# Kernel tuning notes

Hardware: AMD Instinct MI355X
Metric: run time of the kernel (lower is better)

The kernel has to match this reference:

```python
import jax, jax.numpy as jnp
import numpy as np

DIM_MODEL = 1024
NUM_HEADS = 16
DROPOUT_P = 0.5
SCALE = float(np.sqrt(DIM_MODEL // NUM_HEADS))  # NOTE: source MULTIPLIES by this (unusual but faithful)
DROP_KEY = jax.random.key(42)


def setup_inputs() -> dict:
    key = jax.random.key(0)
    ks = jax.random.split(key, 9)
    B, LQ, LK, D = 4, 2048, 2048, DIM_MODEL
    s = 1.0 / np.sqrt(D)
    return {
        "query": jax.random.normal(ks[0], (B, LQ, D), jnp.float32),
        "key": jax.random.normal(ks[1], (B, LK, D), jnp.float32),
        "value": jax.random.normal(ks[2], (B, LK, D), jnp.float32),
        "Wq": jax.random.normal(ks[3], (D, D), jnp.float32) * s,
        "bq": jax.random.normal(ks[4], (D,), jnp.float32) * s,
        "Wk": jax.random.normal(ks[5], (D, D), jnp.float32) * s,
        "bk": jax.random.normal(ks[6], (D,), jnp.float32) * s,
        "Wv": jax.random.normal(ks[7], (D, D), jnp.float32) * s,
        "bv": jax.random.normal(ks[8], (D,), jnp.float32) * s,
    }


def reference(query, key, value, Wq, bq, Wk, bk, Wv, bv):
    # Linear projections (W stored as [in, out])
    q = jnp.einsum('bqd,de->bqe', query, Wq) + bq
    k = jnp.einsum('bkd,de->bke', key, Wk) + bk
    v = jnp.einsum('bkd,de->bke', value, Wv) + bv
    # scores scaled by MULTIPLYING sqrt(d_head), per source
    scores = jnp.einsum('bqe,bke->bqk', q, k) * SCALE
    probs = jax.nn.softmax(scores, axis=-1)
    # dropout (train mode, p=0.5), deterministic fixed key for reproducibility
    keep = jax.random.bernoulli(DROP_KEY, 1.0 - DROPOUT_P, probs.shape)
    probs = jnp.where(keep, probs / (1.0 - DROPOUT_P), 0.0)
    return jnp.einsum('bqk,bke->bqe', probs, v)
```

## Files before the change

kernel.cpp:

```cpp
#include <hip/hip_runtime.h>
#include <math.h>

#define BATCH  4
#define LSEQ   2048
#define DMODEL 1024
#define MROWS  (BATCH * LSEQ)
#define SCORE_SCALE 8.0f

#define THREEFRY_PARTITIONABLE 1

typedef __bf16 bf16_t;
typedef bf16_t bf16x8 __attribute__((ext_vector_type(8)));
typedef bf16_t bf16x4 __attribute__((ext_vector_type(4)));
typedef float  f32x4  __attribute__((ext_vector_type(4)));

#define LDSP(p) ((__attribute__((address_space(3))) void*)(p))
#define GLBP(p) ((const __attribute__((address_space(1))) void*)(p))

__device__ __forceinline__ unsigned rotl32(unsigned x, int r) {
    return (x << r) | (x >> (32 - r));
}

__device__ __forceinline__ void threefry2x32(unsigned k0, unsigned k1,
                                             unsigned x0, unsigned x1,
                                             unsigned& o0, unsigned& o1) {
    const unsigned ks0 = k0, ks1 = k1, ks2 = k0 ^ k1 ^ 0x1BD11BDAu;
    x0 += ks0; x1 += ks1;
#define TF_R(r) { x0 += x1; x1 = rotl32(x1, r); x1 ^= x0; }
    TF_R(13) TF_R(15) TF_R(26) TF_R(6)
    x0 += ks1; x1 += ks2 + 1u;
    TF_R(17) TF_R(29) TF_R(16) TF_R(24)
    x0 += ks2; x1 += ks0 + 2u;
    TF_R(13) TF_R(15) TF_R(26) TF_R(6)
    x0 += ks0; x1 += ks1 + 3u;
    TF_R(17) TF_R(29) TF_R(16) TF_R(24)
    x0 += ks1; x1 += ks2 + 4u;
    TF_R(13) TF_R(15) TF_R(26) TF_R(6)
    x0 += ks2; x1 += ks0 + 5u;
#undef TF_R
    o0 = x0; o1 = x1;
}

__device__ __forceinline__ bool dropout_keep(unsigned n) {
    unsigned o0, o1;
#if THREEFRY_PARTITIONABLE
    threefry2x32(0u, 42u, 0u, n, o0, o1);
    unsigned bits = o0 ^ o1;
#else
    const unsigned HALF = (unsigned)(BATCH * LSEQ) * (unsigned)LSEQ / 2u;
    unsigned c0 = (n < HALF) ? n : (n - HALF);
    unsigned c1 = (n < HALF) ? (n + HALF) : n;
    threefry2x32(0u, 42u, c0, c1, o0, o1);
    unsigned bits = (n < HALF) ? o0 : o1;
#endif
    return bits < 0x80000000u;
}

__global__ __launch_bounds__(256)
void split_f32(const float* __restrict__ X0, const float* __restrict__ X1,
               bf16_t* __restrict__ hi, bf16_t* __restrict__ lo, int n) {
    const int y = blockIdx.y;
    const float* X = y ? X1 : X0;
    long long i = (long long)(blockIdx.x * 256 + threadIdx.x) * 4;
    if (i >= n) return;
    float4 v = *(const float4*)(X + i);
    bf16x4 h, l;
    h[0] = (bf16_t)v.x; l[0] = (bf16_t)(v.x - (float)h[0]);
    h[1] = (bf16_t)v.y; l[1] = (bf16_t)(v.y - (float)h[1]);
    h[2] = (bf16_t)v.z; l[2] = (bf16_t)(v.z - (float)h[2]);
    h[3] = (bf16_t)v.w; l[3] = (bf16_t)(v.w - (float)h[3]);
    *(bf16x4*)(hi + (long long)y * n + i) = h;
    *(bf16x4*)(lo + (long long)y * n + i) = l;
}

__global__ __launch_bounds__(256)
void cvt_bf16(const float* __restrict__ X, bf16_t* __restrict__ Y, int n) {
    long long i = (long long)(blockIdx.x * 256 + threadIdx.x) * 8;
    if (i >= n) return;
    float4 a = *(const float4*)(X + i);
    float4 b = *(const float4*)(X + i + 4);
    bf16x8 o;
    o[0] = (bf16_t)a.x; o[1] = (bf16_t)a.y; o[2] = (bf16_t)a.z; o[3] = (bf16_t)a.w;
    o[4] = (bf16_t)b.x; o[5] = (bf16_t)b.y; o[6] = (bf16_t)b.z; o[7] = (bf16_t)b.w;
    *(bf16x8*)(Y + i) = o;
}

__global__ __launch_bounds__(256)
void split_transpose(const float* __restrict__ W0, const float* __restrict__ W1,
                     bf16_t* __restrict__ Th, bf16_t* __restrict__ Tl,
                     int Kd, int Nd) {
    __shared__ float t[32][33];
    const int z = blockIdx.z;
    const float* W = z ? W1 : W0;
    const long long zo = (long long)z * Kd * Nd;
    const int bx = blockIdx.x * 32;
    const int by = blockIdx.y * 32;
    const int tx = threadIdx.x & 31, ty = threadIdx.x >> 5;
#pragma unroll
    for (int i = 0; i < 4; ++i)
        t[ty + i * 8][tx] = W[(long long)(by + ty + i * 8) * Nd + bx + tx];
    __syncthreads();
#pragma unroll
    for (int i = 0; i < 4; ++i) {
        float v = t[tx][ty + i * 8];
        long long idx = zo + (long long)(bx + ty + i * 8) * Kd + by + tx;
        bf16_t h = (bf16_t)v;
        Th[idx] = h;
        Tl[idx] = (bf16_t)(v - (float)h);
    }
}

template <int SPLIT, int OUT, int BROW>
__global__ __launch_bounds__(256)
void gemm_mfma(const bf16_t* __restrict__ Ah, const bf16_t* __restrict__ Al,
               const bf16_t* __restrict__ Bh, const bf16_t* __restrict__ Bl,
               const float* __restrict__ bias, const float* __restrict__ bias2,
               float* __restrict__ Cf, bf16_t* __restrict__ Ch,
               bf16_t* __restrict__ Cl,
               int M, int N, int K, float scale,
               long long sA, long long sB, long long sC,
               int SX, int NYt) {
    constexpr int TM = 128, TN = 128, TOT = 256, CHUNKS = 4;
    constexpr int NB = SPLIT ? 2 : 1;
    constexpr int BUFSZ = NB * TOT * 32;
    __shared__ __align__(16) bf16_t smem[2 * BUFSZ];

    const int bid = blockIdx.x;
    const int xcd = bid & 7;
    const int ii = bid >> 3;
    const int perz = SX * NYt;
    const int zz = ii / perz;
    const int rr = ii - zz * perz;
    const int nx = xcd + ((rr % SX) << 3);
    const int my = rr / SX;
    const long long z = zz;
    const int m0 = my * TM, n0 = nx * TN;

    const int tid = threadIdx.x;
    const int lane = tid & 63;
    const int wave = tid >> 6;
    const int quad = lane >> 4;
    const int l16 = lane & 15;
    const int wm = (wave & 1) * 64;
    const int wn = (wave >> 1) * 64;

    const bf16_t* gAh = Ah + z * sA;
    const bf16_t* gBh = Bh + z * sB;
    const bf16_t* gAl = SPLIT ? Al + z * sA : nullptr;
    const bf16_t* gBl = SPLIT ? Bl + z * sB : nullptr;

    const int lrow = lane >> 2;
    const int scol = ((lane & 3) ^ ((lrow >> 1) & 3)) * 8;
    const int sw = (l16 >> 1) & 3;

    auto issue = [&](int k0, int b) {
        bf16_t* base = smem + b * BUFSZ;
#pragma unroll
        for (int c = 0; c < CHUNKS; ++c) {
            const int rbase = wave * 64 + c * 16;
            const int row = rbase + lrow;
            if (rbase < TM) {
                const long long g = (long long)(m0 + row) * K + k0 + scol;
                __builtin_amdgcn_global_load_lds(GLBP(gAh + g), LDSP(base + row * 32), 16, 0, 0);
                if constexpr (SPLIT)
                    __builtin_amdgcn_global_load_lds(GLBP(gAl + g), LDSP(base + TOT * 32 + row * 32), 16, 0, 0);
            } else {
                const int br = row - TM;
                const long long g = (long long)(n0 + br) * K + k0 + scol;
                __builtin_amdgcn_global_load_lds(GLBP(gBh + g), LDSP(base + TM * 32 + br * 32), 16, 0, 0);
                if constexpr (SPLIT)
                    __builtin_amdgcn_global_load_lds(GLBP(gBl + g), LDSP(base + TOT * 32 + TM * 32 + br * 32), 16, 0, 0);
            }
        }
    };

    f32x4 acc[4][4];
#pragma unroll
    for (int i = 0; i < 4; ++i)
#pragma unroll
        for (int j = 0; j < 4; ++j)
            acc[i][j] = (f32x4){0.f, 0.f, 0.f, 0.f};

    issue(0, 0);
    const int NIT = K >> 5;
    for (int it = 0; it < NIT; ++it) {
        const int b = it & 1;
        const bool more = (it + 1) < NIT;
        if (more) issue((it + 1) << 5, b ^ 1);
        if constexpr (SPLIT) {
            if (more) asm volatile("s_waitcnt vmcnt(8)" ::: "memory");
            else      asm volatile("s_waitcnt vmcnt(0)" ::: "memory");
        } else {
            if (more) asm volatile("s_waitcnt vmcnt(4)" ::: "memory");
            else      asm volatile("s_waitcnt vmcnt(0)" ::: "memory");
        }
        asm volatile("s_barrier" ::: "memory");

        bf16_t* base = smem + b * BUFSZ;
        bf16_t* sAh = base;
        bf16_t* sBh = base + TM * 32;
        bf16_t* sAl = base + TOT * 32;
        bf16_t* sBl = base + TOT * 32 + TM * 32;

        bf16x8 afh[4], bfh[4], afl[4], bfl[4];
#pragma unroll
        for (int i = 0; i < 4; ++i) {
            const int ao = (wm + i * 16 + l16) * 32 + (quad ^ sw) * 8;
            afh[i] = *(const bf16x8*)(sAh + ao);
            if constexpr (SPLIT) afl[i] = *(const bf16x8*)(sAl + ao);
        }
#pragma unroll
        for (int j = 0; j < 4; ++j) {
            const int bo = (wn + j * 16 + l16) * 32 + (quad ^ sw) * 8;
            bfh[j] = *(const bf16x8*)(sBh + bo);
            if constexpr (SPLIT) bfl[j] = *(const bf16x8*)(sBl + bo);
        }
#pragma unroll
        for (int i = 0; i < 4; ++i)
#pragma unroll
            for (int j = 0; j < 4; ++j) {
                acc[i][j] = __builtin_amdgcn_mfma_f32_16x16x32_bf16(afh[i], bfh[j], acc[i][j], 0, 0, 0);
                if constexpr (SPLIT) {
                    acc[i][j] = __builtin_amdgcn_mfma_f32_16x16x32_bf16(afh[i], bfl[j], acc[i][j], 0, 0, 0);
                    acc[i][j] = __builtin_amdgcn_mfma_f32_16x16x32_bf16(afl[i], bfh[j], acc[i][j], 0, 0, 0);
                }
            }
        asm volatile("s_barrier" ::: "memory");
    }

    const float* bz = (z == 1 && bias2) ? bias2 : bias;
#pragma unroll
    for (int i = 0; i < 4; ++i)
#pragma unroll
        for (int j = 0; j < 4; ++j) {
            const int n = n0 + wn + j * 16 + l16;
            float bvn = 0.f;
            if constexpr (OUT != 0 && !BROW) bvn = bz[n];
#pragma unroll
            for (int r = 0; r < 4; ++r) {
                const int m = m0 + wm + i * 16 + quad * 4 + r;
                const long long idx = z * sC + (long long)m * N + n;
                float v = acc[i][j][r];
                if constexpr (OUT == 0) {
                    Cf[idx] = v * scale;
                } else if constexpr (OUT == 1) {
                    v += bvn;
                    bf16_t h = (bf16_t)v;
                    Ch[idx] = h;
                    Cl[idx] = (bf16_t)(v - (float)h);
                } else {
                    v += BROW ? bz[m] : bvn;
                    Ch[idx] = (bf16_t)v;
                }
            }
        }
}

__global__ __launch_bounds__(256)
void softmax_dropout(const float* __restrict__ S, bf16_t* __restrict__ P) {
    const unsigned row = blockIdx.x;
    const float* rp = S + (long long)row * LSEQ;
    const int tid = threadIdx.x;

    float v[8];
    *(float4*)(v)     = *(const float4*)(rp + tid * 8);
    *(float4*)(v + 4) = *(const float4*)(rp + tid * 8 + 4);

    float m = v[0];
#pragma unroll
    for (int e = 1; e < 8; ++e) m = fmaxf(m, v[e]);
#pragma unroll
    for (int o = 1; o < 64; o <<= 1) m = fmaxf(m, __shfl_xor(m, o));
    __shared__ float redm[4];
    if ((tid & 63) == 0) redm[tid >> 6] = m;
    __syncthreads();
    m = fmaxf(fmaxf(redm[0], redm[1]), fmaxf(redm[2], redm[3]));

    float s = 0.f;
#pragma unroll
    for (int e = 0; e < 8; ++e) { v[e] = __expf(v[e] - m); s += v[e]; }
#pragma unroll
    for (int o = 1; o < 64; o <<= 1) s += __shfl_xor(s, o);
    __shared__ float reds[4];
    if ((tid & 63) == 0) reds[tid >> 6] = s;
    __syncthreads();
    s = (reds[0] + reds[1]) + (reds[2] + reds[3]);

    const float inv = 2.0f / s;
    const unsigned nb = row * (unsigned)LSEQ + (unsigned)(tid * 8);
    bf16x8 o8;
#pragma unroll
    for (int e = 0; e < 8; ++e)
        o8[e] = (bf16_t)(dropout_keep(nb + e) ? v[e] * inv : 0.0f);
    *(bf16x8*)(P + (long long)row * LSEQ + tid * 8) = o8;
}

extern "C" void kernel_launch(void* const* d_in, const int* in_sizes, int n_in,
                              void* d_out, int out_size, void* d_ws, size_t ws_size,
                              hipStream_t stream) {
    const float* query = (const float*)d_in[0];
    const float* key_  = (const float*)d_in[1];
    const float* value = (const float*)d_in[2];
    const float* Wq = (const float*)d_in[3];
    const float* bq = (const float*)d_in[4];
    const float* Wk = (const float*)d_in[5];
    const float* bk = (const float*)d_in[6];
    const float* Wv = (const float*)d_in[7];
    const float* bv = (const float*)d_in[8];
    float* out = (float*)d_out;

    char* w = (char*)d_ws;
    const size_t Q1 = (size_t)MROWS * DMODEL * 2;
    bf16_t* Qh  = (bf16_t*)(w);
    bf16_t* Ql  = (bf16_t*)(w + 2 * Q1);
    bf16_t* VT  = (bf16_t*)(w + 4 * Q1);
    float*  S   = (float*)(w + 5 * Q1);
    bf16_t* XvH  = (bf16_t*)(w + 5 * Q1);
    bf16_t* XqkH = (bf16_t*)(w + 5 * Q1);
    bf16_t* XqkL = (bf16_t*)(w + 7 * Q1);
    bf16_t* WTh = (bf16_t*)(w + 9 * Q1);
    bf16_t* WTl = (bf16_t*)(w + 9 * Q1 + 2 * (size_t)DMODEL * DMODEL * 2);
    bf16_t* P   = Qh;

    dim3 b256(256);
    const int NELEM = MROWS * DMODEL;
    const long long DD = (long long)DMODEL * DMODEL;
    dim3 gwt1(DMODEL / 32, DMODEL / 32, 1);
    dim3 gwt2(DMODEL / 32, DMODEL / 32, 2);

    split_transpose<<<gwt1, b256, 0, stream>>>(Wv, nullptr, WTh, WTl, DMODEL, DMODEL);
    cvt_bf16<<<dim3(NELEM / 2048), b256, 0, stream>>>(value, XvH, NELEM);
    gemm_mfma<0, 2, 1><<<dim3(512), b256, 0, stream>>>(
        WTh, nullptr, XvH, nullptr, bv, nullptr, nullptr, VT, nullptr,
        DMODEL, LSEQ, DMODEL, 1.f,
        0, (long long)LSEQ * DMODEL, (long long)DMODEL * LSEQ,
        2, DMODEL / 128);

    split_transpose<<<gwt2, b256, 0, stream>>>(Wq, Wk, WTh, WTl, DMODEL, DMODEL);
    split_f32<<<dim3(NELEM / 1024, 2), b256, 0, stream>>>(query, key_, XqkH, XqkL, NELEM);
    gemm_mfma<1, 1, 0><<<dim3(1024), b256, 0, stream>>>(
        XqkH, XqkL, WTh, WTl, bq, bk, nullptr, Qh, Ql,
        MROWS, DMODEL, DMODEL, 1.f,
        (long long)NELEM, DD, (long long)NELEM,
        1, MROWS / 128);

    gemm_mfma<1, 0, 0><<<dim3(1024), b256, 0, stream>>>(
        Qh, Ql, Qh + NELEM, Ql + NELEM, nullptr, nullptr, S, nullptr, nullptr,
        LSEQ, LSEQ, DMODEL, SCORE_SCALE,
        (long long)LSEQ * DMODEL, (long long)LSEQ * DMODEL,
        (long long)LSEQ * LSEQ,
        2, LSEQ / 128);

    softmax_dropout<<<dim3(MROWS), b256, 0, stream>>>(S, P);

    gemm_mfma<0, 0, 0><<<dim3(512), b256, 0, stream>>>(
        P, nullptr, VT, nullptr, nullptr, nullptr, out, nullptr, nullptr,
        LSEQ, DMODEL, LSEQ, 1.f,
        (long long)LSEQ * LSEQ, (long long)DMODEL * LSEQ,
        (long long)LSEQ * DMODEL,
        1, LSEQ / 128);
}
```

Before: 478.7 us.

## Add 256x256-tile 8-wave split-bf16 GEMM for QK projection and scores

Adds a new 512-thread GEMM kernel with 256x256 output tiles, double-buffered direct global-to-LDS loads, swizzled LDS layout, and phased MFMA issue with barriers and setprio. It replaces the 128-tile kernel for the Q/K projection and the QK^T score GEMM, both of which use three-term hi/lo bf16 products. Larger tiles raise arithmetic intensity and cut global/LDS traffic per FLOP, and the XCD-aware block remap aims to improve L2 locality. In exchange it needs heavy register use (128 accumulators per thread) and many barriers, and launches only 256 blocks, which may limit occupancy and load balance.

New measurement: 468.8 us. 1.02x faster.

```diff
diff --git a/kernel.cpp b/kernel.cpp
--- a/kernel.cpp
+++ b/kernel.cpp
@@ -256,6 +256,152 @@
         }
 }
 
+template <int OUT>
+__global__ __launch_bounds__(512, 2)
+void gemm_mfma_8ph(const bf16_t* __restrict__ Ah, const bf16_t* __restrict__ Al,
+                   const bf16_t* __restrict__ Bh, const bf16_t* __restrict__ Bl,
+                   const float* __restrict__ bias, const float* __restrict__ bias2,
+                   float* __restrict__ Cf, bf16_t* __restrict__ Ch,
+                   bf16_t* __restrict__ Cl,
+                   int M, int N, int K, float scale,
+                   long long sA, long long sB, long long sC,
+                   int NYt, int NZ) {
+    constexpr int TM = 256, TN = 256;
+    constexpr int PLANE = 256 * 32;
+    __shared__ __align__(16) bf16_t smem[2 * 4 * PLANE];
+
+    const int bid = blockIdx.x;
+    const int gid = (bid & 7) * 32 + (bid >> 3);
+    const int nzy = NZ * NYt;
+    const int nx = gid / nzy;
+    const int rem = gid - nx * nzy;
+    const int zz = rem / NYt;
+    const int my = rem - zz * NYt;
+    const long long z = zz;
+    const int m0 = my * TM, n0 = nx * TN;
+
+    const int tid = threadIdx.x;
+    const int lane = tid & 63;
+    const int wave = tid >> 6;
+    const int quad = lane >> 4;
+    const int l16 = lane & 15;
+    const int wm = (wave >> 2) * 128;
+    const int wn = (wave & 3) * 64;
+
+    const bf16_t* gAh = Ah + z * sA;
+    const bf16_t* gAl = Al + z * sA;
+    const bf16_t* gBh = Bh + z * sB;
+    const bf16_t* gBl = Bl + z * sB;
+
+    const int lrow = lane >> 2;
+    const int scol = ((lane & 3) ^ ((lrow >> 1) & 3)) * 8;
+    const int sw = (l16 >> 1) & 3;
+
+    auto issue = [&](int k0, int b) {
+        bf16_t* base = smem + b * (4 * PLANE);
+#pragma unroll
+        for (int c = 0; c < 8; ++c) {
+            const int s = wave * 8 + c;
+            const int p = s >> 4;
+            const int row = ((s & 15) << 4) + lrow;
+            bf16_t* dst = base + p * PLANE + row * 32;
+            const long long ka = (long long)(m0 + row) * K + k0 + scol;
+            const long long kb = (long long)(n0 + row) * K + k0 + scol;
+            if (p == 0)
+                __builtin_amdgcn_global_load_lds(GLBP(gAh + ka), LDSP(dst), 16, 0, 0);
+            else if (p == 1)
+                __builtin_amdgcn_global_load_lds(GLBP(gBh + kb), LDSP(dst), 16, 0, 0);
+            else if (p == 2)
+                __builtin_amdgcn_global_load_lds(GLBP(gAl + ka), LDSP(dst), 16, 0, 0);
+            else
+                __builtin_amdgcn_global_load_lds(GLBP(gBl + kb), LDSP(dst), 16, 0, 0);
+        }
+    };
+
+    f32x4 acc[8][4];
+#pragma unroll
+    for (int i = 0; i < 8; ++i)
+#pragma unroll
+        for (int j = 0; j < 4; ++j)
+            acc[i][j] = (f32x4){0.f, 0.f, 0.f, 0.f};
+
+    issue(0, 0);
+    const int NIT = K >> 5;
+    for (int it = 0; it < NIT; ++it) {
+        const int b = it & 1;
+        const bool more = (it + 1) < NIT;
+        if (more) issue((it + 1) << 5, b ^ 1);
+        if (more) asm volatile("s_waitcnt vmcnt(8)" ::: "memory");
+        else      asm volatile("s_waitcnt vmcnt(0)" ::: "memory");
+        asm volatile("s_barrier" ::: "memory");
+
+        bf16_t* base = smem + b * (4 * PLANE);
+        bf16_t* sAh = base;
+        bf16_t* sBh = base + PLANE;
+        bf16_t* sAl = base + 2 * PLANE;
+        bf16_t* sBl = base + 3 * PLANE;
+
+        bf16x8 bfh[4], bfl[4];
+#pragma unroll
+        for (int j = 0; j < 4; ++j) {
+            const int bo = (wn + j * 16 + l16) * 32 + (quad ^ sw) * 8;
+            bfh[j] = *(const bf16x8*)(sBh + bo);
+            bfl[j] = *(const bf16x8*)(sBl + bo);
+        }
+
+#pragma unroll
+        for (int ph = 0; ph < 4; ++ph) {
+            bf16x8 afh[2], afl[2];
+#pragma unroll
+            for (int i = 0; i < 2; ++i) {
+                const int ao = (wm + (ph * 2 + i) * 16 + l16) * 32 + (quad ^ sw) * 8;
+                afh[i] = *(const bf16x8*)(sAh + ao);
+                afl[i] = *(const bf16x8*)(sAl + ao);
+            }
+            asm volatile("s_barrier" ::: "memory");
+            asm volatile("s_waitcnt lgkmcnt(0)" ::: "memory");
+            __builtin_amdgcn_sched_barrier(0);
+            __builtin_amdgcn_s_setprio(1);
+#pragma unroll
+            for (int i = 0; i < 2; ++i)
+#pragma unroll
+                for (int j = 0; j < 4; ++j) {
+                    f32x4 a = acc[ph * 2 + i][j];
+                    a = __builtin_amdgcn_mfma_f32_16x16x32_bf16(afh[i], bfh[j], a, 0, 0, 0);
+                    a = __builtin_amdgcn_mfma_f32_16x16x32_bf16(afh[i], bfl[j], a, 0, 0, 0);
+                    a = __builtin_amdgcn_mfma_f32_16x16x32_bf16(afl[i], bfh[j], a, 0, 0, 0);
+                    acc[ph * 2 + i][j] = a;
+                }
+            __builtin_amdgcn_s_setprio(0);
+            asm volatile("s_barrier" ::: "memory");
+        }
+    }
+
+    const float* bz = (z == 1 && bias2) ? bias2 : bias;
+#pragma unroll
+    for (int i = 0; i < 8; ++i)
+#pragma unroll
+        for (int j = 0; j < 4; ++j) {
+            const int n = n0 + wn + j * 16 + l16;
+            float bvn = 0.f;
+            if constexpr (OUT != 0) bvn = bz[n];
+#pragma unroll
+            for (int r = 0; r < 4; ++r) {
+                const int m = m0 + wm + i * 16 + quad * 4 + r;
+                const long long idx = z * sC + (long long)m * N + n;
+                float v = acc[i][j][r];
+                if constexpr (OUT == 0) {
+                    Cf[idx] = v * scale;
+                } else {
+                    v += bvn;
+                    bf16_t h = (bf16_t)v;
+                    Ch[idx] = h;
+                    Cl[idx] = (bf16_t)(v - (float)h);
+                }
+            }
+        }
+}
+
 __global__ __launch_bounds__(256)
 void softmax_dropout(const float* __restrict__ S, bf16_t* __restrict__ P) {
     const unsigned row = blockIdx.x;
@@ -323,6 +469,7 @@
     bf16_t* P   = Qh;
 
     dim3 b256(256);
+    dim3 b512(512);
     const int NELEM = MROWS * DMODEL;
     const long long DD = (long long)DMODEL * DMODEL;
     dim3 gwt1(DMODEL / 32, DMODEL / 32, 1);
@@ -338,18 +485,18 @@
 
     split_transpose<<<gwt2, b256, 0, stream>>>(Wq, Wk, WTh, WTl, DMODEL, DMODEL);
     split_f32<<<dim3(NELEM / 1024, 2), b256, 0, stream>>>(query, key_, XqkH, XqkL, NELEM);
-    gemm_mfma<1, 1, 0><<<dim3(1024), b256, 0, stream>>>(
+    gemm_mfma_8ph<1><<<dim3(256), b512, 0, stream>>>(
         XqkH, XqkL, WTh, WTl, bq, bk, nullptr, Qh, Ql,
         MROWS, DMODEL, DMODEL, 1.f,
         (long long)NELEM, DD, (long long)NELEM,
-        1, MROWS / 128);
-
-    gemm_mfma<1, 0, 0><<<dim3(1024), b256, 0, stream>>>(
+        MROWS / 256, 2);
+
+    gemm_mfma_8ph<0><<<dim3(256), b512, 0, stream>>>(
         Qh, Ql, Qh + NELEM, Ql + NELEM, nullptr, nullptr, S, nullptr, nullptr,
         LSEQ, LSEQ, DMODEL, SCORE_SCALE,
         (long long)LSEQ * DMODEL, (long long)LSEQ * DMODEL,
         (long long)LSEQ * LSEQ,
-        2, LSEQ / 128);
+        LSEQ / 256, 4);
 
     softmax_dropout<<<dim3(MROWS), b256, 0, stream>>>(S, P);
 
```
